# Optimization experiments

Measured on AMD Instinct MI355X. Metric: run time of the kernel, lower is better.

Reference implementation:

```python
import jax, jax.numpy as jnp
import numpy as np

COMMITMENT_COST = 0.25

def setup_inputs() -> dict:
    key = jax.random.key(0)
    k1, k2 = jax.random.split(key)
    inputs = jax.random.normal(k1, (64, 256, 32, 32), dtype=jnp.float32)
    emb_w = jax.random.normal(k2, (1024, 256), dtype=jnp.float32)
    return {"inputs": inputs, "emb_w": emb_w}

def reference(inputs, emb_w):
    # inputs: [B, C, H, W] with C == embedding_dim; emb_w: [K, D]
    K, D = emb_w.shape
    x = jnp.transpose(inputs, (0, 2, 3, 1))          # [B, H, W, D]
    flat = x.reshape(-1, D)                          # [N, D]
    distances = (jnp.sum(flat * flat, axis=1, keepdims=True)
                 + jnp.sum(emb_w * emb_w, axis=1)
                 - 2.0 * flat @ emb_w.T)
    idx = jnp.argmin(distances, axis=1)              # [N]
    encodings = jax.nn.one_hot(idx, K, dtype=flat.dtype)  # [N, K]
    quantized = emb_w[idx].reshape(x.shape)          # gather == onehot @ emb_w
    # eval-mode forward (no EMA buffer mutation)
    loss = COMMITMENT_COST * jnp.mean((jax.lax.stop_gradient(quantized) - x) ** 2)
    quantized_st = x + jax.lax.stop_gradient(quantized - x)  # straight-through
    avg_probs = jnp.mean(encodings, axis=0)
    perplexity = jnp.exp(-jnp.sum(avg_probs * jnp.log(avg_probs + 1e-10)))
    return (loss, jnp.transpose(quantized_st, (0, 3, 1, 2)), perplexity, encodings)
```

## Files before the change

kernel.cpp:

```cpp
#include <hip/hip_runtime.h>

typedef _Float16 f16;
typedef _Float16 f16x4 __attribute__((ext_vector_type(4)));
typedef _Float16 f16x8 __attribute__((ext_vector_type(8)));
typedef float f32x4 __attribute__((ext_vector_type(4)));
typedef float f32x16 __attribute__((ext_vector_type(16)));
typedef unsigned u32;
typedef u32 u32x4 __attribute__((ext_vector_type(4)));

constexpr int Dd = 256;
constexpr long long QOFF     = 1;
constexpr long long PERP_OFF = 16777217LL;
constexpr long long ENC_OFF  = 16777218LL;
constexpr long long ENC_CNT  = 67108864LL;

__device__ inline f32x4 ntload4(const float* p) {
    return __builtin_nontemporal_load(reinterpret_cast<const f32x4*>(p));
}

__global__ void prep_kernel(const float* __restrict__ emb, char* __restrict__ epk,
                            float* __restrict__ enorm) {
    const int t = threadIdx.x;
    const int k = blockIdx.x * 4 + (t >> 6);
    const int d4 = (t & 63) * 4;
    float4 v = *reinterpret_cast<const float4*>(emb + (size_t)k * Dd + d4);
    float s = v.x * v.x + v.y * v.y + v.z * v.z + v.w * v.w;
#pragma unroll
    for (int m = 1; m < 64; m <<= 1) s += __shfl_xor(s, m);
    float a[4] = {v.x, v.y, v.z, v.w};
    f16x4 h;
#pragma unroll
    for (int j = 0; j < 4; ++j) h[j] = (f16)a[j];
    const int kt = k >> 5, l31 = k & 31;
    const int dc = d4 >> 4, hb = (d4 >> 3) & 1, j0 = d4 & 7;
    const int lane = 32 * hb + l31;
    size_t off = (size_t)kt * 16384 + (size_t)dc * 1024 + lane * 16 + j0 * 2;
    *reinterpret_cast<f16x4*>(epk + off) = h;
    if ((t & 63) == 0) enorm[k] = s;
}

__global__ __launch_bounds__(512, 4) void argmin_kernel(
    const float* __restrict__ in, const char* __restrict__ epk,
    const float* __restrict__ enorm, float* __restrict__ gout)
{
    __shared__ char lds[40960];
    float* mb1 = reinterpret_cast<float*>(lds + 32768);
    float* mb2 = reinterpret_cast<float*>(lds + 34816);
    int*   mi1 = reinterpret_cast<int*>(lds + 36864);
    int*   mi2 = reinterpret_cast<int*>(lds + 38912);

    const int t  = threadIdx.x;
    const int g  = blockIdx.x & 3;
    const int pb = blockIdx.x >> 2;
    const int n0 = pb * 512;

    const int lane = t & 63, w = t >> 6;
    const int l31 = lane & 31, hh = lane >> 5;
    const int kt = g * 8 + w;
    const int kb = kt * 32;

    f16x8 e[16];
    {
        const char* pe = epk + (size_t)kt * 16384 + lane * 16;
#pragma unroll
        for (int dc = 0; dc < 16; ++dc)
            e[dc] = *reinterpret_cast<const f16x8*>(pe + dc * 1024);
    }
    const int pxor = (l31 & 15) << 4;

    const int sc  = t & 15;
    const int sdp = t >> 4;
    const int sdpe = sdp ^ sc;

#pragma unroll 1
    for (int ch = 0; ch < 8; ++ch) {
        const int nc = n0 + ch * 64;
        const int b = nc >> 10, hw0 = nc & 1023;
        const float* inb = in + (size_t)b * (Dd * 1024) + hw0;

#pragma unroll 1
        for (int it = 0; it < 4; ++it) {
            const int d = (it * 32 + sdpe) * 2;
            f32x4 v0 = ntload4(inb + (size_t)d * 1024 + sc * 4);
            f32x4 v1 = ntload4(inb + (size_t)(d + 1) * 1024 + sc * 4);
#pragma unroll
            for (int j = 0; j < 4; ++j) {
                int p = 4 * sc + j;
                union { f16 h[2]; u32 u; } ph;
                ph.h[0] = (f16)v0[j]; ph.h[1] = (f16)v1[j];
                int off = (p * 512 + d * 2) ^ ((p & 15) << 4);
                *reinterpret_cast<u32*>(lds + off) = ph.u;
            }
        }
        __syncthreads();

#pragma unroll 1
        for (int tl = 0; tl < 2; ++tl) {
            f32x16 acc = (f32x16)(0.f);
            const int xrow = (tl * 32 + l31) * 512;
#pragma unroll
            for (int dc = 0; dc < 16; ++dc) {
                f16x8 xh = *reinterpret_cast<const f16x8*>(
                    lds + xrow + ((dc * 32 + hh * 16) ^ pxor));
                acc = __builtin_amdgcn_mfma_f32_32x32x16_f16(e[dc], xh, acc, 0, 0, 0);
            }
            float bd1 = 3.4e38f, bd2 = 3.4e38f; int bi1 = 0, bi2 = 0;
#pragma unroll
            for (int rq = 0; rq < 4; ++rq) {
                float4 env = *reinterpret_cast<const float4*>(enorm + kb + 8 * rq + 4 * hh);
                float en4[4] = {env.x, env.y, env.z, env.w};
#pragma unroll
                for (int ri = 0; ri < 4; ++ri) {
                    float s = fmaf(-2.0f, acc[rq * 4 + ri], en4[ri]);
                    int k = kb + 8 * rq + 4 * hh + ri;
                    if (s < bd1) { bd2 = bd1; bi2 = bi1; bd1 = s; bi1 = k; }
                    else if (s < bd2) { bd2 = s; bi2 = k; }
                }
            }
            {
                float ob1 = __shfl_xor(bd1, 32); int oi1 = __shfl_xor(bi1, 32);
                float ob2 = __shfl_xor(bd2, 32); int oi2 = __shfl_xor(bi2, 32);
                if (ob1 < bd1 || (ob1 == bd1 && oi1 < bi1)) {
                    float nb2; int ni2;
                    if (bd1 < ob2 || (bd1 == ob2 && bi1 < oi2)) { nb2 = bd1; ni2 = bi1; }
                    else { nb2 = ob2; ni2 = oi2; }
                    bd1 = ob1; bi1 = oi1; bd2 = nb2; bi2 = ni2;
                } else if (ob1 < bd2 || (ob1 == bd2 && oi1 < bi2)) { bd2 = ob1; bi2 = oi1; }
            }
            if (hh == 0) {
                int s = w * 64 + tl * 32 + l31;
                mb1[s] = bd1; mb2[s] = bd2; mi1[s] = bi1; mi2[s] = bi2;
            }
        }
        __syncthreads();

        if (t < 64) {
            float b1 = mb1[t], b2 = mb2[t]; int i1 = mi1[t], i2 = mi2[t];
#pragma unroll
            for (int ww = 1; ww < 8; ++ww) {
                int s = ww * 64 + t;
                float ob1 = mb1[s], ob2 = mb2[s]; int oi1 = mi1[s], oi2 = mi2[s];
                if (ob1 < b1 || (ob1 == b1 && oi1 < i1)) {
                    float nb2; int ni2;
                    if (b1 < ob2 || (b1 == ob2 && i1 < oi2)) { nb2 = b1; ni2 = i1; }
                    else { nb2 = ob2; ni2 = oi2; }
                    b1 = ob1; i1 = oi1; b2 = nb2; i2 = ni2;
                } else if (ob1 < b2 || (ob1 == b2 && oi1 < i2)) { b2 = ob1; i2 = oi1; }
            }
            f32x4 o;
            o[0] = b1; o[1] = b2;
            o[2] = __int_as_float(i1); o[3] = __int_as_float(i2);
            __builtin_nontemporal_store(
                o, reinterpret_cast<f32x4*>(gout + ((size_t)g * 65536 + nc + t) * 4));
        }
        __syncthreads();
    }
}

__global__ __launch_bounds__(256) void quantref_kernel(
    const float* __restrict__ in, const float* __restrict__ emb,
    const float* __restrict__ enorm, const float* __restrict__ gout,
    int* __restrict__ idx_out, float* __restrict__ outq,
    float* __restrict__ partials, int* __restrict__ counts)
{
    __shared__ float red[2][4][64];
    __shared__ int rowsel[64];
    __shared__ float sred[4];
    const int t = threadIdx.x;
    const int p = t & 63, cq = t >> 6;
    const int n0 = blockIdx.x * 64;
    const int b = n0 >> 10, hw0 = n0 & 1023;

    int k0, k1;
    {
        f32x4 v0 = *reinterpret_cast<const f32x4*>(gout + (size_t)(n0 + p) * 4);
        float b1 = v0[0], b2 = v0[1];
        int i1 = __float_as_int(v0[2]), i2 = __float_as_int(v0[3]);
#pragma unroll
        for (int g = 1; g < 4; ++g) {
            f32x4 v = *reinterpret_cast<const f32x4*>(
                gout + ((size_t)g * 65536 + n0 + p) * 4);
            float c1 = v[0], c2 = v[1];
            int j1 = __float_as_int(v[2]), j2 = __float_as_int(v[3]);
            if (c1 < b1 || (c1 == b1 && j1 < i1)) {
                float nb2; int ni2;
                if (b1 < c2 || (b1 == c2 && i1 < j2)) { nb2 = b1; ni2 = i1; }
                else { nb2 = c2; ni2 = j2; }
                b2 = nb2; i2 = ni2; b1 = c1; i1 = j1;
            } else if (c1 < b2 || (c1 == b2 && j1 < i2)) {
                b2 = c1; i2 = j1;
            }
        }
        k0 = i1; k1 = i2;
    }

    const float* e0 = emb + (size_t)k0 * Dd + cq * 64;
    const float* e1 = emb + (size_t)k1 * Dd + cq * 64;
    const float* xb = in + (size_t)b * (Dd * 1024) + (size_t)(cq * 64) * 1024 + hw0 + p;

    float xr[64];
    float d0 = 0.f, d1 = 0.f;
#pragma unroll
    for (int c = 0; c < 64; c += 4) {
        float4 a0 = *reinterpret_cast<const float4*>(e0 + c);
        float4 a1 = *reinterpret_cast<const float4*>(e1 + c);
        xr[c + 0] = __builtin_nontemporal_load(xb + (size_t)(c + 0) * 1024);
        xr[c + 1] = __builtin_nontemporal_load(xb + (size_t)(c + 1) * 1024);
        xr[c + 2] = __builtin_nontemporal_load(xb + (size_t)(c + 2) * 1024);
        xr[c + 3] = __builtin_nontemporal_load(xb + (size_t)(c + 3) * 1024);
        d0 = fmaf(xr[c+3], a0.w, fmaf(xr[c+2], a0.z, fmaf(xr[c+1], a0.y, fmaf(xr[c+0], a0.x, d0))));
        d1 = fmaf(xr[c+3], a1.w, fmaf(xr[c+2], a1.z, fmaf(xr[c+1], a1.y, fmaf(xr[c+0], a1.x, d1))));
    }
    red[0][cq][p] = d0;
    red[1][cq][p] = d1;
    __syncthreads();
    if (t < 64) {
        float dot0 = (red[0][0][t] + red[0][1][t]) + (red[0][2][t] + red[0][3][t]);
        float dot1 = (red[1][0][t] + red[1][1][t]) + (red[1][2][t] + red[1][3][t]);
        float s0 = enorm[k0] - 2.f * dot0;
        float s1 = enorm[k1] - 2.f * dot1;
        int row = (s1 < s0 || (s1 == s0 && k1 < k0)) ? k1 : k0;
        rowsel[t] = row;
        idx_out[n0 + t] = row;
        atomicAdd(&counts[row], 1);
    }
    __syncthreads();

    const int row = rowsel[p];
    const float* erow = emb + (size_t)row * Dd + cq * 64;
    const size_t base = (size_t)b * (Dd * 1024) + (size_t)(cq * 64) * 1024 + hw0 + p;
    float ls = 0.f;
#pragma unroll
    for (int c = 0; c < 64; c += 4) {
        float4 ev = *reinterpret_cast<const float4*>(erow + c);
        float e4[4] = {ev.x, ev.y, ev.z, ev.w};
#pragma unroll
        for (int j = 0; j < 4; ++j) {
            size_t a = base + (size_t)(c + j) * 1024;
            __builtin_nontemporal_store(e4[j], outq + a);
            float df = e4[j] - xr[c + j];
            ls = fmaf(df, df, ls);
        }
    }
#pragma unroll
    for (int m = 1; m < 64; m <<= 1) ls += __shfl_xor(ls, m);
    if ((t & 63) == 0) sred[t >> 6] = ls;
    __syncthreads();
    if (t == 0) partials[blockIdx.x] = (sred[0] + sred[1]) + (sred[2] + sred[3]);
}

__global__ void enc_kernel(const int* __restrict__ idx, float* __restrict__ enc) {
    const long long T = 16777215LL;
    long long gid    = (long long)blockIdx.x * 256 + threadIdx.x;
    long long stride = (long long)gridDim.x * 256;
    if (gid == 0) {
        enc[0] = (idx[0] == 0) ? 1.f : 0.f;
        enc[1] = (idx[0] == 1) ? 1.f : 0.f;
        enc[67108862LL] = (idx[65535] == 1022) ? 1.f : 0.f;
        enc[67108863LL] = (idx[65535] == 1023) ? 1.f : 0.f;
    }
    for (long long c = gid; c < T; c += stride) {
        long long rel = 2 + 4 * c;
        int n  = (int)(rel >> 10);
        int kk = (int)(rel & 1023);
        f32x4 v;
        if (kk <= 1020) {
            int iv = idx[n];
            v[0] = (kk     == iv) ? 1.f : 0.f;
            v[1] = (kk + 1 == iv) ? 1.f : 0.f;
            v[2] = (kk + 2 == iv) ? 1.f : 0.f;
            v[3] = (kk + 3 == iv) ? 1.f : 0.f;
        } else {
#pragma unroll
            for (int j = 0; j < 4; ++j) {
                long long rr = rel + j;
                int nn = (int)(rr >> 10);
                int kj = (int)(rr & 1023);
                v[j] = (idx[nn] == kj) ? 1.f : 0.f;
            }
        }
        __builtin_nontemporal_store(v, reinterpret_cast<f32x4*>(enc + rel));
    }
}

__global__ __launch_bounds__(1024) void fin_kernel(
    const int* __restrict__ counts, const float* __restrict__ partials,
    float* __restrict__ out)
{
    __shared__ float r1[16];
    __shared__ float r2[16];
    const int t = threadIdx.x;
    float pl = partials[t];
    float pv = (float)counts[t] * (1.0f / 65536.0f);
    float pp = pv * logf(pv + 1e-10f);
#pragma unroll
    for (int m = 1; m < 64; m <<= 1) {
        pl += __shfl_xor(pl, m);
        pp += __shfl_xor(pp, m);
    }
    if ((t & 63) == 0) { r1[t >> 6] = pl; r2[t >> 6] = pp; }
    __syncthreads();
    if (t == 0) {
        float s1 = 0.f, s2 = 0.f;
#pragma unroll
        for (int i = 0; i < 16; ++i) { s1 += r1[i]; s2 += r2[i]; }
        out[0]        = 0.25f * s1 / 16777216.0f;
        out[PERP_OFF] = expf(-s2);
    }
}

extern "C" void kernel_launch(void* const* d_in, const int* in_sizes, int n_in,
                              void* d_out, int out_size, void* d_ws, size_t ws_size,
                              hipStream_t stream) {
    const float* in  = (const float*)d_in[0];
    const float* emb = (const float*)d_in[1];
    float* out = (float*)d_out;

    char* ws = (char*)d_ws;
    int*   counts   = (int*)ws;
    float* partials = (float*)(ws + 4096);
    int*   idx      = (int*)(ws + 16384);

    const size_t goutB = 4194304, epkB = 524288;
    const size_t tailBytes = goutB + epkB + 4096;
    uintptr_t base = ((uintptr_t)(out + ENC_OFF + ENC_CNT) - tailBytes) & ~(uintptr_t)255;
    float* gout  = (float*)base;
    char*  epk   = (char*)(base + goutB);
    float* enorm = (float*)(base + goutB + epkB);

    (void)hipMemsetAsync(counts, 0, 4096, stream);
    prep_kernel<<<256, 256, 0, stream>>>(emb, epk, enorm);
    argmin_kernel<<<512, 512, 0, stream>>>(in, epk, enorm, gout);
    quantref_kernel<<<1024, 256, 0, stream>>>(in, emb, enorm, gout, idx,
                                              out + QOFF, partials, counts);
    enc_kernel<<<8192, 256, 0, stream>>>(idx, out + ENC_OFF);
    fin_kernel<<<1, 1024, 0, stream>>>(counts, partials, out);
}
```

Before: 257.8 us.

## Prefetch next input chunk into registers while computing the current chunk in argmin

The argmin kernel now software-pipelines its input loads. Global loads for the next 64-pixel chunk are issued into a register buffer before the current chunk's MFMA and argmin work. After that work the buffer is converted to f16 and written to LDS. This is meant to hide global-load latency behind compute instead of stalling at the start of each chunk. It adds 32 VGPRs of staging under a 4-blocks-per-CU launch bound, which risks register spills or lower occupancy.

Measured after the change: 402.4 us. 56.1% more time.

```diff
diff --git a/kernel.cpp b/kernel.cpp
--- a/kernel.cpp
+++ b/kernel.cpp
@@ -38,6 +38,35 @@
     *reinterpret_cast<f16x4*>(epk + off) = h;
     if ((t & 63) == 0) enorm[k] = s;
 }
+
+#define ARG_ISSUE(CH)                                                          \
+    {                                                                          \
+        const int nc_ = n0 + (CH) * 64;                                        \
+        const float* inb_ = in + (size_t)(nc_ >> 10) * (Dd * 1024) + (nc_ & 1023); \
+        _Pragma("unroll")                                                      \
+        for (int it = 0; it < 4; ++it) {                                       \
+            const int d_ = it * 64 + dbase;                                    \
+            rg[2 * it]     = ntload4(inb_ + (size_t)d_ * 1024 + sc * 4);       \
+            rg[2 * it + 1] = ntload4(inb_ + (size_t)(d_ + 1) * 1024 + sc * 4); \
+        }                                                                      \
+    }
+
+#define ARG_WRITE_LDS()                                                        \
+    {                                                                          \
+        _Pragma("unroll")                                                      \
+        for (int it = 0; it < 4; ++it) {                                       \
+            const int d_ = it * 64 + dbase;                                    \
+            _Pragma("unroll")                                                  \
+            for (int j = 0; j < 4; ++j) {                                      \
+                int p_ = 4 * sc + j;                                           \
+                union { f16 h[2]; u32 u; } ph_;                                \
+                ph_.h[0] = (f16)rg[2 * it][j];                                 \
+                ph_.h[1] = (f16)rg[2 * it + 1][j];                             \
+                int off_ = (p_ * 512 + d_ * 2) ^ ((p_ & 15) << 4);             \
+                *reinterpret_cast<u32*>(lds + off_) = ph_.u;                   \
+            }                                                                  \
+        }                                                                      \
+    }
 
 __global__ __launch_bounds__(512, 4) void argmin_kernel(
     const float* __restrict__ in, const char* __restrict__ epk,
@@ -70,29 +99,18 @@
 
     const int sc  = t & 15;
     const int sdp = t >> 4;
-    const int sdpe = sdp ^ sc;
+    const int dbase = (sdp ^ sc) * 2;
+
+    f32x4 rg[8];
+
+    ARG_ISSUE(0);
+    ARG_WRITE_LDS();
+    ARG_ISSUE(1);
+    __syncthreads();
 
 #pragma unroll 1
     for (int ch = 0; ch < 8; ++ch) {
         const int nc = n0 + ch * 64;
-        const int b = nc >> 10, hw0 = nc & 1023;
-        const float* inb = in + (size_t)b * (Dd * 1024) + hw0;
-
-#pragma unroll 1
-        for (int it = 0; it < 4; ++it) {
-            const int d = (it * 32 + sdpe) * 2;
-            f32x4 v0 = ntload4(inb + (size_t)d * 1024 + sc * 4);
-            f32x4 v1 = ntload4(inb + (size_t)(d + 1) * 1024 + sc * 4);
-#pragma unroll
-            for (int j = 0; j < 4; ++j) {
-                int p = 4 * sc + j;
-                union { f16 h[2]; u32 u; } ph;
-                ph.h[0] = (f16)v0[j]; ph.h[1] = (f16)v1[j];
-                int off = (p * 512 + d * 2) ^ ((p & 15) << 4);
-                *reinterpret_cast<u32*>(lds + off) = ph.u;
-            }
-        }
-        __syncthreads();
 
 #pragma unroll 1
         for (int tl = 0; tl < 2; ++tl) {
@@ -152,6 +170,10 @@
             o[2] = __int_as_float(i1); o[3] = __int_as_float(i2);
             __builtin_nontemporal_store(
                 o, reinterpret_cast<f32x4*>(gout + ((size_t)g * 65536 + nc + t) * 4));
+        }
+        if (ch < 7) {
+            ARG_WRITE_LDS();
+            if (ch < 6) ARG_ISSUE(ch + 2);
         }
         __syncthreads();
     }
```

## Pre-pack inputs to fp16 MFMA layout in a separate kernel before argmin

Applied to the files above, without the earlier changes.

Adds an xprep kernel that converts the NCHW fp32 input into fp16 tiles already arranged in MFMA fragment order, written to scratch inside the output buffer. The argmin kernel then copies these packed tiles linearly into LDS and reads them without swizzling. Previously each of the four codebook-group blocks re-read and converted the same fp32 input. The change trades that repeated fp32 reading and conversion for one extra kernel launch and a 32 MB write plus reread of the packed data.

Result: faster. 247.1 us (-4.1%).

```diff
diff --git a/kernel.cpp b/kernel.cpp
--- a/kernel.cpp
+++ b/kernel.cpp
@@ -39,8 +39,47 @@
     if ((t & 63) == 0) enorm[k] = s;
 }
 
+__global__ __launch_bounds__(256) void xprep_kernel(const float* __restrict__ in,
+                                                    char* __restrict__ xpk) {
+    __shared__ char lds[32768];
+    const int t = threadIdx.x;
+    const int n0 = blockIdx.x * 64;
+    const int b = n0 >> 10, hw0 = n0 & 1023;
+    const float* inb = in + (size_t)b * (Dd * 1024) + hw0;
+    {
+        const int c  = t & 15;
+        const int g  = (t >> 4) & 3;
+        const int hi = t >> 6;
+        const int dp = hi * 4 + (g ^ (c >> 2));
+        for (int it = 0; it < 8; ++it) {
+            const int d = it * 32 + dp * 2;
+            f32x4 v0 = ntload4(inb + (size_t)d * 1024 + c * 4);
+            f32x4 v1 = ntload4(inb + (size_t)(d + 1) * 1024 + c * 4);
+#pragma unroll
+            for (int j = 0; j < 4; ++j) {
+                int p = 4 * c + j;
+                union { f16 h[2]; u32 u; } ph;
+                ph.h[0] = (f16)v0[j]; ph.h[1] = (f16)v1[j];
+                int off = (p * 512 + d * 2) ^ ((p & 15) << 4);
+                *reinterpret_cast<u32*>(lds + off) = ph.u;
+            }
+        }
+    }
+    __syncthreads();
+    char* outb = xpk + (size_t)n0 * 512;
+    for (int it = 0; it < 8; ++it) {
+        int fid = it * 256 + t;
+        int lane = fid & 63, dcl = (fid >> 6) & 15, ptl = fid >> 10;
+        int p  = ptl * 32 + (lane & 31);
+        int d0 = dcl * 16 + (lane >> 5) * 8;
+        int off = (p * 512 + d0 * 2) ^ ((p & 15) << 4);
+        u32x4 v = *reinterpret_cast<const u32x4*>(lds + off);
+        __builtin_nontemporal_store(v, reinterpret_cast<u32x4*>(outb + (size_t)fid * 16));
+    }
+}
+
 __global__ __launch_bounds__(512, 4) void argmin_kernel(
-    const float* __restrict__ in, const char* __restrict__ epk,
+    const char* __restrict__ xpk, const char* __restrict__ epk,
     const float* __restrict__ enorm, float* __restrict__ gout)
 {
     __shared__ char lds[40960];
@@ -66,30 +105,18 @@
         for (int dc = 0; dc < 16; ++dc)
             e[dc] = *reinterpret_cast<const f16x8*>(pe + dc * 1024);
     }
-    const int pxor = (l31 & 15) << 4;
-
-    const int sc  = t & 15;
-    const int sdp = t >> 4;
-    const int sdpe = sdp ^ sc;
 
 #pragma unroll 1
     for (int ch = 0; ch < 8; ++ch) {
         const int nc = n0 + ch * 64;
-        const int b = nc >> 10, hw0 = nc & 1023;
-        const float* inb = in + (size_t)b * (Dd * 1024) + hw0;
-
-#pragma unroll 1
-        for (int it = 0; it < 4; ++it) {
-            const int d = (it * 32 + sdpe) * 2;
-            f32x4 v0 = ntload4(inb + (size_t)d * 1024 + sc * 4);
-            f32x4 v1 = ntload4(inb + (size_t)(d + 1) * 1024 + sc * 4);
-#pragma unroll
-            for (int j = 0; j < 4; ++j) {
-                int p = 4 * sc + j;
-                union { f16 h[2]; u32 u; } ph;
-                ph.h[0] = (f16)v0[j]; ph.h[1] = (f16)v1[j];
-                int off = (p * 512 + d * 2) ^ ((p & 15) << 4);
-                *reinterpret_cast<u32*>(lds + off) = ph.u;
+
+        {
+            const char* xsrc = xpk + (size_t)nc * 512;
+#pragma unroll
+            for (int i = 0; i < 4; ++i) {
+                u32x4 v = __builtin_nontemporal_load(
+                    reinterpret_cast<const u32x4*>(xsrc + (size_t)(i * 512 + t) * 16));
+                *reinterpret_cast<u32x4*>(lds + (i * 512 + t) * 16) = v;
             }
         }
         __syncthreads();
@@ -97,11 +124,10 @@
 #pragma unroll 1
         for (int tl = 0; tl < 2; ++tl) {
             f32x16 acc = (f32x16)(0.f);
-            const int xrow = (tl * 32 + l31) * 512;
+            const int xbase = tl * 16384 + lane * 16;
 #pragma unroll
             for (int dc = 0; dc < 16; ++dc) {
-                f16x8 xh = *reinterpret_cast<const f16x8*>(
-                    lds + xrow + ((dc * 32 + hh * 16) ^ pxor));
+                f16x8 xh = *reinterpret_cast<const f16x8*>(lds + xbase + dc * 1024);
                 acc = __builtin_amdgcn_mfma_f32_32x32x16_f16(e[dc], xh, acc, 0, 0, 0);
             }
             float bd1 = 3.4e38f, bd2 = 3.4e38f; int bi1 = 0, bi2 = 0;
@@ -321,16 +347,18 @@
     float* partials = (float*)(ws + 4096);
     int*   idx      = (int*)(ws + 16384);
 
-    const size_t goutB = 4194304, epkB = 524288;
-    const size_t tailBytes = goutB + epkB + 4096;
+    const size_t xpkB = 33554432, goutB = 4194304, epkB = 524288;
+    const size_t tailBytes = xpkB + goutB + epkB + 4096;
     uintptr_t base = ((uintptr_t)(out + ENC_OFF + ENC_CNT) - tailBytes) & ~(uintptr_t)255;
-    float* gout  = (float*)base;
-    char*  epk   = (char*)(base + goutB);
-    float* enorm = (float*)(base + goutB + epkB);
+    char*  xpk   = (char*)base;
+    float* gout  = (float*)(base + xpkB);
+    char*  epk   = (char*)(base + xpkB + goutB);
+    float* enorm = (float*)(base + xpkB + goutB + epkB);
 
     (void)hipMemsetAsync(counts, 0, 4096, stream);
     prep_kernel<<<256, 256, 0, stream>>>(emb, epk, enorm);
-    argmin_kernel<<<512, 512, 0, stream>>>(in, epk, enorm, gout);
+    xprep_kernel<<<1024, 256, 0, stream>>>(in, xpk);
+    argmin_kernel<<<512, 512, 0, stream>>>(xpk, epk, enorm, gout);
     quantref_kernel<<<1024, 256, 0, stream>>>(in, emb, enorm, gout, idx,
                                               out + QOFF, partials, counts);
     enc_kernel<<<8192, 256, 0, stream>>>(idx, out + ENC_OFF);
```
